# Performance work log

Measured on AMD Instinct MI355X. Metric: run time of the kernel, lower is better.

## Reference

```python
import jax, jax.numpy as jnp
import numpy as np

B, L, D = 1, 4096, 1024
H = 16
HD = D // H
SCALE = HD ** -0.5


def setup_inputs() -> dict:
    key = jax.random.key(0)
    k1, k2, k3 = jax.random.split(key, 3)
    X = jax.random.normal(k1, (B, L, D), dtype=jnp.float32)
    # torch Linear default init ~ U(-1/sqrt(fan_in), 1/sqrt(fan_in)); scaled normals are fine for a reference
    Wqkv = jax.random.normal(k2, (D, 3 * D), dtype=jnp.float32) * (D ** -0.5)
    bqkv = jnp.zeros((3 * D,), dtype=jnp.float32)
    Wproj = jax.random.normal(k3, (D, D), dtype=jnp.float32) * (D ** -0.5)
    bproj = jnp.zeros((D,), dtype=jnp.float32)
    return {"X": X, "Wqkv": Wqkv, "bqkv": bqkv, "Wproj": Wproj, "bproj": bproj}


def reference(X, Wqkv, bqkv, Wproj, bproj):
    Bn, Ln, Dn = X.shape
    qkv = X @ Wqkv + bqkv                       # [B, L, 3D]
    qkv = qkv.reshape(Bn, Ln, 3, H, HD)
    q, k, v = qkv[:, :, 0], qkv[:, :, 1], qkv[:, :, 2]   # [B, L, H, HD]
    # attention scores [B, H, L, L] (naive, matches original)
    attn = jnp.einsum('bqhd,bkhd->bhqk', q, k) * SCALE
    causal = jnp.tril(jnp.ones((Ln, Ln), dtype=bool))     # True = keep
    attn = jnp.where(causal, attn, -jnp.inf)
    score = jax.nn.softmax(attn, axis=-1)
    out = jnp.einsum('bhqk,bkhd->bqhd', score, v)         # [B, L, H, HD]
    out = out.reshape(Bn, Ln, Dn)
    return out @ Wproj + bproj
```

## Files before the change

kernel.cpp:

```cpp
#include <hip/hip_runtime.h>
#include <hip/hip_bf16.h>
#include <string.h>


typedef unsigned short ushort_t;
typedef __attribute__((ext_vector_type(8))) short short8;
typedef __attribute__((ext_vector_type(4))) float f32x4;

#define MFMA16(a, b, c) __builtin_amdgcn_mfma_f32_16x16x32_bf16(a, b, c, 0, 0, 0)

static constexpr int Lq = 4096;
static constexpr int Dm = 1024;
static constexpr int NH = 16;
static constexpr int HD = 64;
static constexpr int D3 = 3072;
static constexpr float SCALE_LOG2E = 0.125f * 1.44269504088896340736f;

__device__ __forceinline__ ushort_t f2bf(float f) {
    union { float f; unsigned int u; } x{f};
    unsigned int u = x.u;
    u += 0x7fffu + ((u >> 16) & 1u);
    return (ushort_t)(u >> 16);
}

__device__ __forceinline__ unsigned int cvtpk(float a, float b) {
    __hip_bfloat162 h = __float22bfloat162_rn(make_float2(a, b));
    unsigned int u;
    memcpy(&u, &h, 4);
    return u;
}

__device__ __forceinline__ void gl2lds16(const ushort_t* g, ushort_t* l) {
    __builtin_amdgcn_global_load_lds(
        (const __attribute__((address_space(1))) unsigned int*)g,
        (__attribute__((address_space(3))) unsigned int*)l, 16, 0, 0);
}

__global__ void __launch_bounds__(256)
prep(const float* __restrict__ X, const float* __restrict__ Wqkv,
     const float* __restrict__ Wproj, ushort_t* __restrict__ Xb,
     ushort_t* __restrict__ WqkvT, ushort_t* __restrict__ WprojT) {
    __shared__ float tile[32][33];
    const int bid = blockIdx.x, tid = threadIdx.x;
    if (bid < 4096) {
        int i = (bid * 256 + tid) * 4;
        float4 v = *(const float4*)&X[i];
        ushort_t r[4] = { f2bf(v.x), f2bf(v.y), f2bf(v.z), f2bf(v.w) };
        *(uint2*)&Xb[i] = *(uint2*)r;
        return;
    }
    const float* W; ushort_t* Wt; int Nd, nb, kb;
    if (bid < 7168) {
        int b = bid - 4096; W = Wqkv;  Wt = WqkvT;  Nd = 3072;
        nb = (b % 96) * 32; kb = (b / 96) * 32;
    } else {
        int b = bid - 7168; W = Wproj; Wt = WprojT; Nd = 1024;
        nb = (b % 32) * 32; kb = (b / 32) * 32;
    }
    const int tx = tid & 31, ty = tid >> 5;
    for (int j = 0; j < 32; j += 8)
        tile[ty + j][tx] = W[(size_t)(kb + ty + j) * Nd + nb + tx];
    __syncthreads();
    for (int j = 0; j < 32; j += 8)
        Wt[(size_t)(nb + ty + j) * Dm + kb + tx] = f2bf(tile[tx][ty + j]);
}

__global__ void __launch_bounds__(256)
gemm_qkv(const ushort_t* __restrict__ A, const ushort_t* __restrict__ Bt,
         const float* __restrict__ bias, ushort_t* __restrict__ Cq,
         ushort_t* __restrict__ Vt) {
    __shared__ alignas(16) ushort_t Alds[128 * 32];
    __shared__ alignas(16) ushort_t Blds[128 * 32];
    const int tid  = threadIdx.x;
    const int lane = tid & 63;
    const int w    = tid >> 6;
    const int quad = lane >> 4;
    const int l16  = lane & 15;
    const int mbase = blockIdx.x * 128;
    const int nbase = blockIdx.y * 128;
    const int moff  = (w >> 1) * 64;
    const int noff  = (w & 1) * 64;
    const int K = Dm;

    f32x4 acc[4][4] = {};

    for (int kb = 0; kb < K; kb += 32) {
        __syncthreads();
        #pragma unroll
        for (int c = 0; c < 2; c++) {
            int id  = w * 128 + c * 64 + lane;
            int row = id >> 2, col = (id & 3) * 8;
            gl2lds16(&A[(size_t)(mbase + row) * K + kb + col], &Alds[(size_t)(w * 128 + c * 64) * 8]);
            gl2lds16(&Bt[(size_t)(nbase + row) * K + kb + col], &Blds[(size_t)(w * 128 + c * 64) * 8]);
        }
        __syncthreads();
        short8 a[4], b[4];
        #pragma unroll
        for (int m = 0; m < 4; m++)
            a[m] = *(const short8*)&Alds[(moff + m * 16 + l16) * 32 + quad * 8];
        #pragma unroll
        for (int n = 0; n < 4; n++)
            b[n] = *(const short8*)&Blds[(noff + n * 16 + l16) * 32 + quad * 8];
        #pragma unroll
        for (int m = 0; m < 4; m++)
            #pragma unroll
            for (int n = 0; n < 4; n++)
                acc[m][n] = MFMA16(a[m], b[n], acc[m][n]);
    }

    if (nbase < 2048) {
        const bool qscale = (nbase < 1024);
        #pragma unroll
        for (int m = 0; m < 4; m++)
            #pragma unroll
            for (int n = 0; n < 4; n++)
                #pragma unroll
                for (int r = 0; r < 4; r++) {
                    int row = mbase + moff + m * 16 + quad * 4 + r;
                    int col = nbase + noff + n * 16 + l16;
                    float v = acc[m][n][r] + bias[col];
                    if (qscale) v *= SCALE_LOG2E;
                    Cq[(size_t)row * D3 + col] = f2bf(v);
                }
    } else {
        #pragma unroll
        for (int m = 0; m < 4; m++)
            #pragma unroll
            for (int r = 0; r < 4; r++) {
                const int key = mbase + moff + m * 16 + quad * 4 + r;
                const int cp  = (key & ~63) + ((key & 15) * 4 + ((key >> 4) & 3));
                #pragma unroll
                for (int n = 0; n < 4; n++) {
                    const int col = nbase + noff + n * 16 + l16;
                    float v = acc[m][n][r] + bias[col];
                    Vt[(size_t)(col - 2048) * Lq + cp] = f2bf(v);
                }
            }
    }
}

__global__ void __launch_bounds__(512, 2)
attn_fwd(const ushort_t* __restrict__ qkv, const ushort_t* __restrict__ Vt,
         ushort_t* __restrict__ O) {
    __shared__ alignas(16) ushort_t Kl[2][2][64 * 64];
    __shared__ alignas(16) ushort_t Vl[2][2][64 * 64];
    __shared__ alignas(16) ushort_t Pl[8 * 32 * 72];
    __shared__ alignas(16) float    Ml[256 * 41];

    const int tid  = threadIdx.x;
    const int lane = tid & 63;
    const int w    = tid >> 6;
    const int half = w >> 2;
    const int sub  = w & 3;
    const int quad = lane >> 4;
    const int l16  = lane & 15;
    const int bid  = blockIdx.x;
    const int h    = bid & 15;
    const int p    = bid >> 4;
    ushort_t* pw   = Pl + w * 32 * 72;
    const float NEG_INF = -__builtin_inff();
    const int sw   = l16 & 7;

    const short bf1 = (short)0x3F80;
    const short8 ones = { bf1, bf1, bf1, bf1, bf1, bf1, bf1, bf1 };

    const ushort_t* kbase = qkv + Dm + h * HD;
    const ushort_t* vbase = Vt + (size_t)h * HD * Lq;

    int kvo[4][2];
    #pragma unroll
    for (int s = 0; s < 4; s++)
        #pragma unroll
        for (int kh = 0; kh < 2; kh++)
            kvo[s][kh] = (s * 16 + l16) * 64 + (((kh * 4 + quad) ^ sw) * 8);

    const int rr = tid >> 3, cc = (tid & 7) ^ (rr & 7);
    const ushort_t* kse = kbase + (size_t)rr * D3 + cc * 8;
    const ushort_t* vse = vbase + (size_t)rr * Lq + cc * 8;
    const int dstoff = w * 512;

    for (int sel = 0; sel < 2; sel++) {
        const int c      = sel ? (31 - p) : p;
        const int qc     = c * 128;
        const int rounds = c + 1;
        const int qw     = qc + sub * 32;

        short8 qf[2][2];
        #pragma unroll
        for (int m = 0; m < 2; m++) {
            const ushort_t* qr = qkv + (size_t)(qw + m * 16 + l16) * D3 + h * HD;
            qf[m][0] = *(const short8*)(qr + quad * 8);
            qf[m][1] = *(const short8*)(qr + 32 + quad * 8);
        }

        f32x4 o[2][4] = {};
        f32x4 lacc[2] = {};

        const ushort_t* kp = kse;
        const ushort_t* vp = vse;

        auto stage = [&](int b) {
            gl2lds16(kp,           &Kl[0][b][dstoff]);
            gl2lds16(kp + 64 * D3, &Kl[1][b][dstoff]);
            gl2lds16(vp,           &Vl[0][b][dstoff]);
            gl2lds16(vp + 64,      &Vl[1][b][dstoff]);
            kp += (size_t)128 * D3;
            vp += 128;
        };

        stage(0);

        for (int r = 0; r < rounds; r++) {
            const int buf = r & 1;
            __syncthreads();
            if (r + 1 < rounds) stage(buf ^ 1);

            const ushort_t* Kb = &Kl[half][buf][0];
            const ushort_t* Vb = &Vl[half][buf][0];
            const int k0 = (2 * r + half) * 64;
            const bool domask = (r == rounds - 1);

            short8 kf[4][2];
            #pragma unroll
            for (int s = 0; s < 4; s++)
                #pragma unroll
                for (int kh = 0; kh < 2; kh++)
                    kf[s][kh] = *(const short8*)&Kb[kvo[s][kh]];

            f32x4 st[2][4];
            #pragma unroll
            for (int m = 0; m < 2; m++)
                #pragma unroll
                for (int s = 0; s < 4; s++) {
                    f32x4 t = {};
                    t = MFMA16(qf[m][0], kf[s][0], t);
                    t = MFMA16(qf[m][1], kf[s][1], t);
                    st[m][s] = t;
                }

            #pragma unroll
            for (int m = 0; m < 2; m++)
                #pragma unroll
                for (int r4 = 0; r4 < 4; r4++) {
                    float e[4];
                    #pragma unroll
                    for (int s = 0; s < 4; s++) {
                        float v = st[m][s][r4];
                        if (domask) {
                            const int qg = qw + m * 16 + quad * 4 + r4;
                            if (k0 + s * 16 + l16 > qg) v = NEG_INF;
                        }
                        e[s] = __builtin_amdgcn_exp2f(v);
                    }
                    uint2 pk = { cvtpk(e[0], e[1]), cvtpk(e[2], e[3]) };
                    *(uint2*)&pw[(m * 16 + quad * 4 + r4) * 72 + l16 * 4] = pk;
                }

            short8 pf[2][2];
            #pragma unroll
            for (int m = 0; m < 2; m++)
                #pragma unroll
                for (int kh = 0; kh < 2; kh++)
                    pf[m][kh] = *(const short8*)&pw[(m * 16 + l16) * 72 + kh * 32 + quad * 8];
            #pragma unroll
            for (int m = 0; m < 2; m++) {
                lacc[m] = MFMA16(pf[m][0], ones, lacc[m]);
                lacc[m] = MFMA16(pf[m][1], ones, lacc[m]);
            }

            short8 vf[4][2];
            #pragma unroll
            for (int t = 0; t < 4; t++)
                #pragma unroll
                for (int kh = 0; kh < 2; kh++)
                    vf[t][kh] = *(const short8*)&Vb[kvo[t][kh]];
            #pragma unroll
            for (int m = 0; m < 2; m++)
                #pragma unroll
                for (int t = 0; t < 4; t++) {
                    o[m][t] = MFMA16(pf[m][0], vf[t][0], o[m][t]);
                    o[m][t] = MFMA16(pf[m][1], vf[t][1], o[m][t]);
                }
        }

        __syncthreads();
        if (half == 1) {
            float* dst = Ml + (sub * 64 + lane) * 41;
            #pragma unroll
            for (int m = 0; m < 2; m++)
                #pragma unroll
                for (int t = 0; t < 4; t++)
                    *(f32x4*)(dst + m * 16 + t * 4) = o[m][t];
            *(f32x4*)(dst + 32) = lacc[0];
            *(f32x4*)(dst + 36) = lacc[1];
        }
        __syncthreads();
        if (half == 0) {
            const float* src = Ml + (sub * 64 + lane) * 41;
            #pragma unroll
            for (int m = 0; m < 2; m++)
                #pragma unroll
                for (int t = 0; t < 4; t++)
                    o[m][t] += *(const f32x4*)(src + m * 16 + t * 4);
            lacc[0] += *(const f32x4*)(src + 32);
            lacc[1] += *(const f32x4*)(src + 36);
            #pragma unroll
            for (int m = 0; m < 2; m++)
                #pragma unroll
                for (int r4 = 0; r4 < 4; r4++) {
                    const float inv = 1.0f / lacc[m][r4];
                    ushort_t* orow = O + (size_t)(qw + m * 16 + quad * 4 + r4) * Dm + h * HD;
                    #pragma unroll
                    for (int t = 0; t < 4; t++)
                        orow[t * 16 + l16] = f2bf(o[m][t][r4] * inv);
                }
        }
        __syncthreads();
    }
}

__global__ void __launch_bounds__(256)
gemm_proj(const ushort_t* __restrict__ A, const ushort_t* __restrict__ Bt,
          const float* __restrict__ bias, float* __restrict__ C) {
    __shared__ alignas(16) ushort_t Alds[128 * 32];
    __shared__ alignas(16) ushort_t Blds[64 * 32];
    const int tid  = threadIdx.x;
    const int lane = tid & 63;
    const int w    = tid >> 6;
    const int quad = lane >> 4;
    const int l16  = lane & 15;
    const int mbase = blockIdx.x * 128;
    const int nbase = blockIdx.y * 64;
    const int moff  = (w >> 1) * 64;
    const int noff  = (w & 1) * 32;
    const int K = Dm, N = Dm;

    f32x4 acc[4][2] = {};

    for (int kb = 0; kb < K; kb += 32) {
        __syncthreads();
        #pragma unroll
        for (int c = 0; c < 2; c++) {
            int id  = w * 128 + c * 64 + lane;
            int row = id >> 2, col = (id & 3) * 8;
            gl2lds16(&A[(size_t)(mbase + row) * K + kb + col], &Alds[(size_t)(w * 128 + c * 64) * 8]);
        }
        {
            int id  = w * 64 + lane;
            int row = id >> 2, col = (id & 3) * 8;
            gl2lds16(&Bt[(size_t)(nbase + row) * K + kb + col], &Blds[(size_t)(w * 64) * 8]);
        }
        __syncthreads();
        short8 a[4], b[2];
        #pragma unroll
        for (int m = 0; m < 4; m++)
            a[m] = *(const short8*)&Alds[(moff + m * 16 + l16) * 32 + quad * 8];
        #pragma unroll
        for (int n = 0; n < 2; n++)
            b[n] = *(const short8*)&Blds[(noff + n * 16 + l16) * 32 + quad * 8];
        #pragma unroll
        for (int m = 0; m < 4; m++)
            #pragma unroll
            for (int n = 0; n < 2; n++)
                acc[m][n] = MFMA16(a[m], b[n], acc[m][n]);
    }

    #pragma unroll
    for (int m = 0; m < 4; m++)
        #pragma unroll
        for (int n = 0; n < 2; n++)
            #pragma unroll
            for (int r = 0; r < 4; r++) {
                int row = mbase + moff + m * 16 + quad * 4 + r;
                int col = nbase + noff + n * 16 + l16;
                C[(size_t)row * N + col] = acc[m][n][r] + bias[col];
            }
}

extern "C" void kernel_launch(void* const* d_in, const int* in_sizes, int n_in,
                              void* d_out, int out_size, void* d_ws, size_t ws_size,
                              hipStream_t stream) {
    const float* X     = (const float*)d_in[0];
    const float* Wqkv  = (const float*)d_in[1];
    const float* bqkv  = (const float*)d_in[2];
    const float* Wproj = (const float*)d_in[3];
    const float* bproj = (const float*)d_in[4];
    float* out = (float*)d_out;

    ushort_t* ws     = (ushort_t*)d_ws;
    ushort_t* Xb     = ws;
    ushort_t* WqkvT  = Xb + (size_t)Lq * Dm;
    ushort_t* WprojT = WqkvT + (size_t)D3 * Dm;
    ushort_t* qkvB   = WprojT + (size_t)Dm * Dm;
    ushort_t* VtB    = qkvB + (size_t)Lq * D3;
    ushort_t* Ob     = VtB + (size_t)NH * HD * Lq;

    prep<<<dim3(8192), 256, 0, stream>>>(X, Wqkv, Wproj, Xb, WqkvT, WprojT);

    gemm_qkv<<<dim3(Lq / 128, D3 / 128), 256, 0, stream>>>(
        Xb, WqkvT, bqkv, qkvB, VtB);

    attn_fwd<<<dim3(256), 512, 0, stream>>>(qkvB, VtB, Ob);

    gemm_proj<<<dim3(Lq / 128, Dm / 64), 256, 0, stream>>>(
        Ob, WprojT, bproj, out);
}
```

Before: 214.4 us.

## Restructure causal attention into one query chunk per 256-thread block

Replaces the 512-thread blocks, which each handled a pair of query chunks with two wave halves splitting the keys and then merging partials through shared memory, with 512 blocks of 256 threads that each own a single 128-row query chunk and walk all its key tiles. Blocks are ordered heaviest-first so the causal workload imbalance is absorbed by the scheduler. This removes the cross-half LDS reduction and its extra barriers and shrinks shared memory per block, which could allow more resident blocks. In exchange, each wave walks twice as many key tiles serially, and per-block load balancing now depends on hardware dispatch rather than explicit pairing.

```diff
diff --git a/kernel.cpp b/kernel.cpp
--- a/kernel.cpp
+++ b/kernel.cpp
@@ -139,24 +139,24 @@
     }
 }
 
-__global__ void __launch_bounds__(512, 2)
+__global__ void __launch_bounds__(256, 2)
 attn_fwd(const ushort_t* __restrict__ qkv, const ushort_t* __restrict__ Vt,
          ushort_t* __restrict__ O) {
-    __shared__ alignas(16) ushort_t Kl[2][2][64 * 64];
-    __shared__ alignas(16) ushort_t Vl[2][2][64 * 64];
-    __shared__ alignas(16) ushort_t Pl[8 * 32 * 72];
-    __shared__ alignas(16) float    Ml[256 * 41];
+    __shared__ alignas(16) ushort_t Kl[2][64 * 64];
+    __shared__ alignas(16) ushort_t Vl[2][64 * 64];
+    __shared__ alignas(16) ushort_t Pl[4 * 32 * 72];
 
     const int tid  = threadIdx.x;
     const int lane = tid & 63;
     const int w    = tid >> 6;
-    const int half = w >> 2;
-    const int sub  = w & 3;
     const int quad = lane >> 4;
     const int l16  = lane & 15;
     const int bid  = blockIdx.x;
     const int h    = bid & 15;
-    const int p    = bid >> 4;
+    const int j    = bid >> 4;
+    const int c    = (bid < 256) ? (31 - j) : (j - 16);
+    const int qw   = c * 128 + w * 32;
+    const int nt   = 2 * c + 2;
     ushort_t* pw   = Pl + w * 32 * 72;
     const float NEG_INF = -__builtin_inff();
     const int sw   = l16 & 7;
@@ -167,6 +167,17 @@
     const ushort_t* kbase = qkv + Dm + h * HD;
     const ushort_t* vbase = Vt + (size_t)h * HD * Lq;
 
+    short8 qf[2][2];
+    #pragma unroll
+    for (int m = 0; m < 2; m++) {
+        const ushort_t* qr = qkv + (size_t)(qw + m * 16 + l16) * D3 + h * HD;
+        qf[m][0] = *(const short8*)(qr + quad * 8);
+        qf[m][1] = *(const short8*)(qr + 32 + quad * 8);
+    }
+
+    f32x4 o[2][4] = {};
+    f32x4 lacc[2] = {};
+
     int kvo[4][2];
     #pragma unroll
     for (int s = 0; s < 4; s++)
@@ -174,149 +185,110 @@
         for (int kh = 0; kh < 2; kh++)
             kvo[s][kh] = (s * 16 + l16) * 64 + (((kh * 4 + quad) ^ sw) * 8);
 
-    const int rr = tid >> 3, cc = (tid & 7) ^ (rr & 7);
-    const ushort_t* kse = kbase + (size_t)rr * D3 + cc * 8;
-    const ushort_t* vse = vbase + (size_t)rr * Lq + cc * 8;
-    const int dstoff = w * 512;
-
-    for (int sel = 0; sel < 2; sel++) {
-        const int c      = sel ? (31 - p) : p;
-        const int qc     = c * 128;
-        const int rounds = c + 1;
-        const int qw     = qc + sub * 32;
-
-        short8 qf[2][2];
-        #pragma unroll
-        for (int m = 0; m < 2; m++) {
-            const ushort_t* qr = qkv + (size_t)(qw + m * 16 + l16) * D3 + h * HD;
-            qf[m][0] = *(const short8*)(qr + quad * 8);
-            qf[m][1] = *(const short8*)(qr + 32 + quad * 8);
-        }
-
-        f32x4 o[2][4] = {};
-        f32x4 lacc[2] = {};
-
-        const ushort_t* kp = kse;
-        const ushort_t* vp = vse;
-
-        auto stage = [&](int b) {
-            gl2lds16(kp,           &Kl[0][b][dstoff]);
-            gl2lds16(kp + 64 * D3, &Kl[1][b][dstoff]);
-            gl2lds16(vp,           &Vl[0][b][dstoff]);
-            gl2lds16(vp + 64,      &Vl[1][b][dstoff]);
-            kp += (size_t)128 * D3;
-            vp += 128;
-        };
-
-        stage(0);
-
-        for (int r = 0; r < rounds; r++) {
-            const int buf = r & 1;
-            __syncthreads();
-            if (r + 1 < rounds) stage(buf ^ 1);
-
-            const ushort_t* Kb = &Kl[half][buf][0];
-            const ushort_t* Vb = &Vl[half][buf][0];
-            const int k0 = (2 * r + half) * 64;
-            const bool domask = (r == rounds - 1);
-
-            short8 kf[4][2];
-            #pragma unroll
-            for (int s = 0; s < 4; s++)
-                #pragma unroll
-                for (int kh = 0; kh < 2; kh++)
-                    kf[s][kh] = *(const short8*)&Kb[kvo[s][kh]];
-
-            f32x4 st[2][4];
-            #pragma unroll
-            for (int m = 0; m < 2; m++)
+    const int gA = w * 64 + lane;
+    const int rA = gA >> 3, cA = (gA & 7) ^ (rA & 7);
+    const int gB = 256 + w * 64 + lane;
+    const int rB = gB >> 3, cB = (gB & 7) ^ (rB & 7);
+    const ushort_t* ksA = kbase + (size_t)rA * D3 + cA * 8;
+    const ushort_t* ksB = kbase + (size_t)rB * D3 + cB * 8;
+    const ushort_t* vsA = vbase + (size_t)rA * Lq + cA * 8;
+    const ushort_t* vsB = vbase + (size_t)rB * Lq + cB * 8;
+    const int dA = w * 512, dB = 2048 + w * 512;
+
+    auto stage = [&](int kt, int b) {
+        const size_t ko = (size_t)kt * 64 * D3;
+        const int    vo = kt * 64;
+        gl2lds16(ksA + ko, &Kl[b][dA]);
+        gl2lds16(ksB + ko, &Kl[b][dB]);
+        gl2lds16(vsA + vo, &Vl[b][dA]);
+        gl2lds16(vsB + vo, &Vl[b][dB]);
+    };
+
+    stage(0, 0);
+
+    for (int kt = 0; kt < nt; kt++) {
+        const int buf = kt & 1;
+        __syncthreads();
+        if (kt + 1 < nt) stage(kt + 1, buf ^ 1);
+
+        const ushort_t* Kb = &Kl[buf][0];
+        const ushort_t* Vb = &Vl[buf][0];
+        const int k0 = kt * 64;
+        const bool domask = (kt >= 2 * c);
+
+        short8 kf[4][2];
+        #pragma unroll
+        for (int s = 0; s < 4; s++)
+            #pragma unroll
+            for (int kh = 0; kh < 2; kh++)
+                kf[s][kh] = *(const short8*)&Kb[kvo[s][kh]];
+
+        f32x4 st[2][4];
+        #pragma unroll
+        for (int m = 0; m < 2; m++)
+            #pragma unroll
+            for (int s = 0; s < 4; s++) {
+                f32x4 t = {};
+                t = MFMA16(qf[m][0], kf[s][0], t);
+                t = MFMA16(qf[m][1], kf[s][1], t);
+                st[m][s] = t;
+            }
+
+        #pragma unroll
+        for (int m = 0; m < 2; m++)
+            #pragma unroll
+            for (int r4 = 0; r4 < 4; r4++) {
+                float e[4];
                 #pragma unroll
                 for (int s = 0; s < 4; s++) {
-                    f32x4 t = {};
-                    t = MFMA16(qf[m][0], kf[s][0], t);
-                    t = MFMA16(qf[m][1], kf[s][1], t);
-                    st[m][s] = t;
+                    float v = st[m][s][r4];
+                    if (domask) {
+                        const int qg = qw + m * 16 + quad * 4 + r4;
+                        if (k0 + s * 16 + l16 > qg) v = NEG_INF;
+                    }
+                    e[s] = __builtin_amdgcn_exp2f(v);
                 }
-
-            #pragma unroll
-            for (int m = 0; m < 2; m++)
-                #pragma unroll
-                for (int r4 = 0; r4 < 4; r4++) {
-                    float e[4];
-                    #pragma unroll
-                    for (int s = 0; s < 4; s++) {
-                        float v = st[m][s][r4];
-                        if (domask) {
-                            const int qg = qw + m * 16 + quad * 4 + r4;
-                            if (k0 + s * 16 + l16 > qg) v = NEG_INF;
-                        }
-                        e[s] = __builtin_amdgcn_exp2f(v);
-                    }
-                    uint2 pk = { cvtpk(e[0], e[1]), cvtpk(e[2], e[3]) };
-                    *(uint2*)&pw[(m * 16 + quad * 4 + r4) * 72 + l16 * 4] = pk;
-                }
-
-            short8 pf[2][2];
-            #pragma unroll
-            for (int m = 0; m < 2; m++)
-                #pragma unroll
-                for (int kh = 0; kh < 2; kh++)
-                    pf[m][kh] = *(const short8*)&pw[(m * 16 + l16) * 72 + kh * 32 + quad * 8];
-            #pragma unroll
-            for (int m = 0; m < 2; m++) {
-                lacc[m] = MFMA16(pf[m][0], ones, lacc[m]);
-                lacc[m] = MFMA16(pf[m][1], ones, lacc[m]);
-            }
-
-            short8 vf[4][2];
+                uint2 pk = { cvtpk(e[0], e[1]), cvtpk(e[2], e[3]) };
+                *(uint2*)&pw[(m * 16 + quad * 4 + r4) * 72 + l16 * 4] = pk;
+            }
+
+        short8 pf[2][2];
+        #pragma unroll
+        for (int m = 0; m < 2; m++)
+            #pragma unroll
+            for (int kh = 0; kh < 2; kh++)
+                pf[m][kh] = *(const short8*)&pw[(m * 16 + l16) * 72 + kh * 32 + quad * 8];
+        #pragma unroll
+        for (int m = 0; m < 2; m++) {
+            lacc[m] = MFMA16(pf[m][0], ones, lacc[m]);
+            lacc[m] = MFMA16(pf[m][1], ones, lacc[m]);
+        }
+
+        short8 vf[4][2];
+        #pragma unroll
+        for (int t = 0; t < 4; t++)
+            #pragma unroll
+            for (int kh = 0; kh < 2; kh++)
+                vf[t][kh] = *(const short8*)&Vb[kvo[t][kh]];
+        #pragma unroll
+        for (int m = 0; m < 2; m++)
+            #pragma unroll
+            for (int t = 0; t < 4; t++) {
+                o[m][t] = MFMA16(pf[m][0], vf[t][0], o[m][t]);
+                o[m][t] = MFMA16(pf[m][1], vf[t][1], o[m][t]);
+            }
+    }
+
+    #pragma unroll
+    for (int m = 0; m < 2; m++)
+        #pragma unroll
+        for (int r4 = 0; r4 < 4; r4++) {
+            const float inv = 1.0f / lacc[m][r4];
+            ushort_t* orow = O + (size_t)(qw + m * 16 + quad * 4 + r4) * Dm + h * HD;
             #pragma unroll
             for (int t = 0; t < 4; t++)
-                #pragma unroll
-                for (int kh = 0; kh < 2; kh++)
-                    vf[t][kh] = *(const short8*)&Vb[kvo[t][kh]];
-            #pragma unroll
-            for (int m = 0; m < 2; m++)
-                #pragma unroll
-                for (int t = 0; t < 4; t++) {
-                    o[m][t] = MFMA16(pf[m][0], vf[t][0], o[m][t]);
-                    o[m][t] = MFMA16(pf[m][1], vf[t][1], o[m][t]);
-                }
-        }
-
-        __syncthreads();
-        if (half == 1) {
-            float* dst = Ml + (sub * 64 + lane) * 41;
-            #pragma unroll
-            for (int m = 0; m < 2; m++)
-                #pragma unroll
-                for (int t = 0; t < 4; t++)
-                    *(f32x4*)(dst + m * 16 + t * 4) = o[m][t];
-            *(f32x4*)(dst + 32) = lacc[0];
-            *(f32x4*)(dst + 36) = lacc[1];
-        }
-        __syncthreads();
-        if (half == 0) {
-            const float* src = Ml + (sub * 64 + lane) * 41;
-            #pragma unroll
-            for (int m = 0; m < 2; m++)
-                #pragma unroll
-                for (int t = 0; t < 4; t++)
-                    o[m][t] += *(const f32x4*)(src + m * 16 + t * 4);
-            lacc[0] += *(const f32x4*)(src + 32);
-            lacc[1] += *(const f32x4*)(src + 36);
-            #pragma unroll
-            for (int m = 0; m < 2; m++)
-                #pragma unroll
-                for (int r4 = 0; r4 < 4; r4++) {
-                    const float inv = 1.0f / lacc[m][r4];
-                    ushort_t* orow = O + (size_t)(qw + m * 16 + quad * 4 + r4) * Dm + h * HD;
-                    #pragma unroll
-                    for (int t = 0; t < 4; t++)
-                        orow[t * 16 + l16] = f2bf(o[m][t][r4] * inv);
-                }
-        }
-        __syncthreads();
-    }
+                orow[t * 16 + l16] = f2bf(o[m][t][r4] * inv);
+        }
 }
 
 __global__ void __launch_bounds__(256)
@@ -400,7 +372,7 @@
     gemm_qkv<<<dim3(Lq / 128, D3 / 128), 256, 0, stream>>>(
         Xb, WqkvT, bqkv, qkvB, VtB);
 
-    attn_fwd<<<dim3(256), 512, 0, stream>>>(qkvB, VtB, Ob);
+    attn_fwd<<<dim3(512), 256, 0, stream>>>(qkvB, VtB, Ob);
 
     gemm_proj<<<dim3(Lq / 128, Dm / 64), 256, 0, stream>>>(
         Ob, WprojT, bproj, out);
```

Result: slower. 247.7 us (+15.5%).
